# Kernel tuning notes

Hardware: AMD Instinct MI355X
Metric: run time of the kernel (lower is better)

Reference implementation:

```python
import jax, jax.numpy as jnp
import numpy as np

B, BANDS, N, IN_C, F, C = 4096, 5, 30, 512, 128, 9

def setup_inputs() -> dict:
    key = jax.random.key(0)
    ks = jax.random.split(key, 10)
    def glorot(k, shape):
        lim = float(np.sqrt(6.0 / (shape[0] + shape[-1])))
        return jax.random.uniform(k, shape, jnp.float32, -lim, lim)
    return {
        "real": jax.random.normal(ks[0], (B, N, IN_C), jnp.float32),
        "imag": jax.random.normal(ks[1], (B, N, IN_C), jnp.float32),
        "graph": jax.random.normal(ks[2], (B, BANDS, N, N), jnp.float32),
        "W1": glorot(ks[3], (IN_C, F)),
        "b1": jnp.zeros((F,), jnp.float32),
        "W2": glorot(ks[4], (F, F)),
        "b2": jnp.zeros((F,), jnp.float32),
        "Wlin": glorot(ks[5], (F, 1)),
        "blin": jnp.zeros((1,), jnp.float32),
        "Wconv": glorot(ks[6], (C, N)),  # Conv1d(30, C, k=1) weight squeezed
        "bconv": jnp.zeros((C,), jnp.float32),
    }

def _norm_adj(graph):
    # adj = mean over bands; PyG from_scipy_sparse_matrix keeps only the
    # nonzero PATTERN (edge weights are discarded in the original code).
    adj = jnp.mean(graph, axis=1)                       # [B, N, N]
    A = (adj != 0).astype(jnp.float32)
    eye = jnp.eye(A.shape[-1], dtype=jnp.float32)
    A_hat = jnp.where(eye > 0, 1.0, A)                  # add remaining self-loops
    deg = A_hat.sum(-1)                                 # [B, N]
    dinv = jnp.where(deg > 0, jax.lax.rsqrt(deg), 0.0)
    return dinv[..., :, None] * A_hat * dinv[..., None, :]  # D^-1/2 (A+I) D^-1/2

def reference(real, imag, graph, W1, b1, W2, b2, Wlin, blin, Wconv, bconv):
    An = _norm_adj(graph)                               # [B, N, N]
    # GCNConv layer 1: propagate(x @ W) + bias, then ReLU (dropout = eval identity)
    h = jnp.einsum('bnm,bmf->bnf', An, real @ W1) + b1
    h = jax.nn.relu(h)
    # GCNConv layer 2
    h = jnp.einsum('bnm,bmf->bnf', An, h @ W2) + b2
    h = jax.nn.relu(h)
    # lin: [B, N, F] -> [B, N], relu, then Conv1d(30->C, k=1) over length-1 axis
    x = jax.nn.relu((h @ Wlin + blin).squeeze(-1))      # [B, N]
    out = x @ Wconv.T + bconv                           # [B, C]
    return out
```

## Files before the change

kernel.cpp:

```cpp
#include <hip/hip_runtime.h>
#include <cstdint>

#define B_SZ 4096
#define NN   30
#define INC  512
#define FF   128
#define CC   9

__global__ __launch_bounds__(128) void k_norm_adj(const float* __restrict__ graph,
                                                  float* __restrict__ An) {
  __shared__ float Ah[NN * NN];
  __shared__ float dinv[NN];
  const int b = blockIdx.x;
  const float* g = graph + (long)b * 5 * NN * NN;
  for (int e = threadIdx.x; e < NN * NN; e += 128) {
    float s = g[e] + g[e + 900] + g[e + 1800] + g[e + 2700] + g[e + 3600];
    float mean = s * 0.2f;
    int i = e / NN;
    int j = e - i * NN;
    Ah[e] = (mean != 0.0f || i == j) ? 1.0f : 0.0f;
  }
  __syncthreads();
  if (threadIdx.x < NN) {
    float d = 0.f;
#pragma unroll
    for (int j = 0; j < NN; ++j) d += Ah[threadIdx.x * NN + j];
    dinv[threadIdx.x] = (d > 0.f) ? (1.0f / sqrtf(d)) : 0.0f;
  }
  __syncthreads();
  float* ob = An + (long)b * NN * NN;
  for (int e = threadIdx.x; e < NN * NN; e += 128) {
    int i = e / NN;
    int j = e - i * NN;
    ob[e] = Ah[e] * dinv[i] * dinv[j];
  }
}

template <int K>
__global__ __launch_bounds__(256) void k_gemm(const float* __restrict__ A,
                                              const float* __restrict__ B,
                                              float* __restrict__ C) {
  constexpr int BM = 128, BN = 128, BK = 16;
  __shared__ float As[BK][BM + 4];
  __shared__ float Bs[BK][BN + 4];
  const int tid = threadIdx.x;
  const int tx = tid & 15;
  const int ty = tid >> 4;
  const long m0 = (long)blockIdx.x * BM;

  float acc[8][8];
#pragma unroll
  for (int i = 0; i < 8; ++i)
#pragma unroll
    for (int j = 0; j < 8; ++j) acc[i][j] = 0.f;

  for (int k0 = 0; k0 < K; k0 += BK) {
#pragma unroll
    for (int it = 0; it < 2; ++it) {
      int idx = tid + 256 * it;
      int arow = idx >> 2;
      int akq = idx & 3;
      float4 av = *(const float4*)(A + (m0 + arow) * (long)K + k0 + akq * 4);
      As[akq * 4 + 0][arow] = av.x;
      As[akq * 4 + 1][arow] = av.y;
      As[akq * 4 + 2][arow] = av.z;
      As[akq * 4 + 3][arow] = av.w;
      int brow = idx >> 5;
      int bc4 = idx & 31;
      float4 bv = *(const float4*)(B + (long)(k0 + brow) * BN + bc4 * 4);
      *(float4*)&Bs[brow][bc4 * 4] = bv;
    }
    __syncthreads();
#pragma unroll
    for (int k = 0; k < BK; ++k) {
      float4 a0 = *(const float4*)&As[k][ty * 8];
      float4 a1 = *(const float4*)&As[k][ty * 8 + 4];
      float4 b0 = *(const float4*)&Bs[k][tx * 4];
      float4 b1 = *(const float4*)&Bs[k][64 + tx * 4];
      float a[8] = {a0.x, a0.y, a0.z, a0.w, a1.x, a1.y, a1.z, a1.w};
      float b[8] = {b0.x, b0.y, b0.z, b0.w, b1.x, b1.y, b1.z, b1.w};
#pragma unroll
      for (int i = 0; i < 8; ++i)
#pragma unroll
        for (int j = 0; j < 8; ++j) acc[i][j] = fmaf(a[i], b[j], acc[i][j]);
    }
    __syncthreads();
  }

#pragma unroll
  for (int i = 0; i < 8; ++i) {
    long row = m0 + ty * 8 + i;
    float4 lo = make_float4(acc[i][0], acc[i][1], acc[i][2], acc[i][3]);
    float4 hi = make_float4(acc[i][4], acc[i][5], acc[i][6], acc[i][7]);
    *(float4*)(C + row * BN + tx * 4) = lo;
    *(float4*)(C + row * BN + 64 + tx * 4) = hi;
  }
}

__global__ __launch_bounds__(128) void k_prop1(const float* __restrict__ An,
                                               const float* __restrict__ Y,
                                               const float* __restrict__ b1,
                                               float* __restrict__ H1) {
  const int b = blockIdx.x;
  const int f = threadIdx.x;
  const float* Yb = Y + (long)b * NN * FF + f;
  float y[NN];
#pragma unroll
  for (int m = 0; m < NN; ++m) y[m] = Yb[m * FF];
  const float* Ab = An + (long)b * NN * NN;
  const float bias = b1[f];
  float* Hb = H1 + (long)b * NN * FF + f;
#pragma unroll 1
  for (int i = 0; i < NN; ++i) {
    float acc = bias;
#pragma unroll
    for (int m = 0; m < NN; ++m) acc = fmaf(Ab[i * NN + m], y[m], acc);
    Hb[i * FF] = fmaxf(acc, 0.f);
  }
}

__global__ __launch_bounds__(128) void k_final(const float* __restrict__ An,
                                               const float* __restrict__ T,
                                               const float* __restrict__ b2,
                                               const float* __restrict__ Wlin,
                                               const float* __restrict__ blin,
                                               const float* __restrict__ Wconv,
                                               const float* __restrict__ bconv,
                                               float* __restrict__ out) {
  __shared__ float partial[2][NN];
  __shared__ float xs[NN];
  const int b = blockIdx.x;
  const int f = threadIdx.x;
  const int wave = f >> 6;
  const int lane = f & 63;
  const float* Tb = T + (long)b * NN * FF + f;
  float t[NN];
#pragma unroll
  for (int m = 0; m < NN; ++m) t[m] = Tb[m * FF];
  const float* Ab = An + (long)b * NN * NN;
  const float bias = b2[f];
  const float wl = Wlin[f];
#pragma unroll 1
  for (int i = 0; i < NN; ++i) {
    float acc = bias;
#pragma unroll
    for (int m = 0; m < NN; ++m) acc = fmaf(Ab[i * NN + m], t[m], acc);
    float c = fmaxf(acc, 0.f) * wl;
#pragma unroll
    for (int off = 32; off > 0; off >>= 1) c += __shfl_down(c, off, 64);
    if (lane == 0) partial[wave][i] = c;
  }
  __syncthreads();
  if (f < NN) {
    float x = partial[0][f] + partial[1][f] + blin[0];
    xs[f] = fmaxf(x, 0.f);
  }
  __syncthreads();
  if (f < CC) {
    float o = bconv[f];
#pragma unroll
    for (int i = 0; i < NN; ++i) o = fmaf(xs[i], Wconv[f * NN + i], o);
    out[(long)b * CC + f] = o;
  }
}

extern "C" void kernel_launch(void* const* d_in, const int* in_sizes, int n_in,
                              void* d_out, int out_size, void* d_ws, size_t ws_size,
                              hipStream_t stream) {
  const float* real  = (const float*)d_in[0];
  const float* graph = (const float*)d_in[2];
  const float* W1    = (const float*)d_in[3];
  const float* b1    = (const float*)d_in[4];
  const float* W2    = (const float*)d_in[5];
  const float* b2    = (const float*)d_in[6];
  const float* Wlin  = (const float*)d_in[7];
  const float* blin  = (const float*)d_in[8];
  const float* Wconv = (const float*)d_in[9];
  const float* bconv = (const float*)d_in[10];
  float* out = (float*)d_out;

  float* An = (float*)d_ws;
  float* Y  = An + (long)B_SZ * NN * NN;
  float* H1 = Y + (long)B_SZ * NN * FF;
  float* T  = Y;

  const int M = B_SZ * NN;

  k_norm_adj<<<B_SZ, 128, 0, stream>>>(graph, An);
  k_gemm<INC><<<M / 128, 256, 0, stream>>>(real, W1, Y);
  k_prop1<<<B_SZ, 128, 0, stream>>>(An, Y, b1, H1);
  k_gemm<FF><<<M / 128, 256, 0, stream>>>(H1, W2, T);
  k_final<<<B_SZ, 128, 0, stream>>>(An, T, b2, Wlin, blin, Wconv, bconv, out);
}
```

Baseline: 758.1 us.

## Replace FP32 SIMT GEMMs with split-bf16 MFMA GEMMs (3-pass emulated fp32)

Both dense GEMMs move from scalar FMA loops to MFMA bf16 matrix instructions. Each fp32 value is split into high and low bf16 halves, and three MFMA passes (hi*hi, lo*hi, hi*lo) approximate fp32 accuracy. Weights are pre-split and transposed by a small prep kernel each call, while activations are split on the fly when loaded into LDS. This targets the FP32 ALU bound of the large 122880x512x128 GEMM. It adds conversion work and scalar uncoalesced output stores, and gives slightly lower precision than true fp32.

```diff
diff --git a/kernel.cpp b/kernel.cpp
--- a/kernel.cpp
+++ b/kernel.cpp
@@ -6,6 +6,18 @@
 #define INC  512
 #define FF   128
 #define CC   9
+
+typedef short short8 __attribute__((ext_vector_type(8)));
+typedef float f32x4 __attribute__((ext_vector_type(4)));
+typedef unsigned short us4 __attribute__((ext_vector_type(4)));
+
+__device__ inline void split_bf16(float x, unsigned short& hi, unsigned short& lo) {
+  uint32_t bits = __float_as_uint(x);
+  hi = (unsigned short)(bits >> 16);
+  float hif = __uint_as_float(((uint32_t)hi) << 16);
+  float r = x - hif;
+  lo = (unsigned short)(__float_as_uint(r) >> 16);
+}
 
 __global__ __launch_bounds__(128) void k_norm_adj(const float* __restrict__ graph,
                                                   float* __restrict__ An) {
@@ -36,64 +48,107 @@
   }
 }
 
+__global__ __launch_bounds__(256) void k_prep_w(const float* __restrict__ W,
+                                                unsigned short* __restrict__ Wth,
+                                                unsigned short* __restrict__ Wtl,
+                                                int K) {
+  int idx = blockIdx.x * 256 + threadIdx.x;
+  if (idx >= K * FF) return;
+  int k = idx >> 7;
+  int n = idx & 127;
+  unsigned short h, l;
+  split_bf16(W[idx], h, l);
+  Wth[n * K + k] = h;
+  Wtl[n * K + k] = l;
+}
+
 template <int K>
-__global__ __launch_bounds__(256) void k_gemm(const float* __restrict__ A,
-                                              const float* __restrict__ B,
-                                              float* __restrict__ C) {
-  constexpr int BM = 128, BN = 128, BK = 16;
-  __shared__ float As[BK][BM + 4];
-  __shared__ float Bs[BK][BN + 4];
+__global__ __launch_bounds__(256) void k_gemm_mfma(const float* __restrict__ A,
+                                                   const unsigned short* __restrict__ Bth,
+                                                   const unsigned short* __restrict__ Btl,
+                                                   float* __restrict__ C) {
+  constexpr int BK = 32;
+  constexpr int LDT = 48;
+  __shared__ unsigned short Ash[128 * LDT];
+  __shared__ unsigned short Asl[128 * LDT];
+  __shared__ unsigned short Bsh[128 * LDT];
+  __shared__ unsigned short Bsl[128 * LDT];
+
   const int tid = threadIdx.x;
-  const int tx = tid & 15;
-  const int ty = tid >> 4;
-  const long m0 = (long)blockIdx.x * BM;
-
-  float acc[8][8];
-#pragma unroll
-  for (int i = 0; i < 8; ++i)
-#pragma unroll
-    for (int j = 0; j < 8; ++j) acc[i][j] = 0.f;
+  const int wave = tid >> 6;
+  const int lane = tid & 63;
+  const int wrow = (wave >> 1) * 64;
+  const int wcol = (wave & 1) * 64;
+  const int fr = lane & 15;
+  const int fq = lane >> 4;
+  const long m0 = (long)blockIdx.x * 128;
+
+  f32x4 acc[4][4];
+#pragma unroll
+  for (int i = 0; i < 4; ++i)
+#pragma unroll
+    for (int j = 0; j < 4; ++j) acc[i][j] = (f32x4){0.f, 0.f, 0.f, 0.f};
 
   for (int k0 = 0; k0 < K; k0 += BK) {
 #pragma unroll
-    for (int it = 0; it < 2; ++it) {
-      int idx = tid + 256 * it;
-      int arow = idx >> 2;
-      int akq = idx & 3;
-      float4 av = *(const float4*)(A + (m0 + arow) * (long)K + k0 + akq * 4);
-      As[akq * 4 + 0][arow] = av.x;
-      As[akq * 4 + 1][arow] = av.y;
-      As[akq * 4 + 2][arow] = av.z;
-      As[akq * 4 + 3][arow] = av.w;
-      int brow = idx >> 5;
-      int bc4 = idx & 31;
-      float4 bv = *(const float4*)(B + (long)(k0 + brow) * BN + bc4 * 4);
-      *(float4*)&Bs[brow][bc4 * 4] = bv;
+    for (int it = 0; it < 4; ++it) {
+      int f = tid + it * 256;
+      int row = f >> 3;
+      int kq = f & 7;
+      float4 v = *(const float4*)(A + (m0 + row) * (long)K + k0 + kq * 4);
+      us4 h, l;
+      split_bf16(v.x, ((unsigned short*)&h)[0], ((unsigned short*)&l)[0]);
+      split_bf16(v.y, ((unsigned short*)&h)[1], ((unsigned short*)&l)[1]);
+      split_bf16(v.z, ((unsigned short*)&h)[2], ((unsigned short*)&l)[2]);
+      split_bf16(v.w, ((unsigned short*)&h)[3], ((unsigned short*)&l)[3]);
+      *(us4*)(Ash + row * LDT + kq * 4) = h;
+      *(us4*)(Asl + row * LDT + kq * 4) = l;
+    }
+#pragma unroll
+    for (int it = 0; it < 4; ++it) {
+      int f = tid + it * 256;
+      int n = f >> 3;
+      int kq = f & 7;
+      us4 vh = *(const us4*)(Bth + (long)n * K + k0 + kq * 4);
+      us4 vl = *(const us4*)(Btl + (long)n * K + k0 + kq * 4);
+      *(us4*)(Bsh + n * LDT + kq * 4) = vh;
+      *(us4*)(Bsl + n * LDT + kq * 4) = vl;
     }
     __syncthreads();
-#pragma unroll
-    for (int k = 0; k < BK; ++k) {
-      float4 a0 = *(const float4*)&As[k][ty * 8];
-      float4 a1 = *(const float4*)&As[k][ty * 8 + 4];
-      float4 b0 = *(const float4*)&Bs[k][tx * 4];
-      float4 b1 = *(const float4*)&Bs[k][64 + tx * 4];
-      float a[8] = {a0.x, a0.y, a0.z, a0.w, a1.x, a1.y, a1.z, a1.w};
-      float b[8] = {b0.x, b0.y, b0.z, b0.w, b1.x, b1.y, b1.z, b1.w};
-#pragma unroll
-      for (int i = 0; i < 8; ++i)
-#pragma unroll
-        for (int j = 0; j < 8; ++j) acc[i][j] = fmaf(a[i], b[j], acc[i][j]);
+
+    short8 bh[4], bl[4];
+#pragma unroll
+    for (int ct = 0; ct < 4; ++ct) {
+      int n = wcol + ct * 16 + fr;
+      bh[ct] = *(const short8*)(Bsh + n * LDT + fq * 8);
+      bl[ct] = *(const short8*)(Bsl + n * LDT + fq * 8);
+    }
+#pragma unroll
+    for (int rt = 0; rt < 4; ++rt) {
+      int m = wrow + rt * 16 + fr;
+      short8 ah = *(const short8*)(Ash + m * LDT + fq * 8);
+      short8 al = *(const short8*)(Asl + m * LDT + fq * 8);
+#pragma unroll
+      for (int ct = 0; ct < 4; ++ct) {
+        acc[rt][ct] = __builtin_amdgcn_mfma_f32_16x16x32_bf16(ah, bh[ct], acc[rt][ct], 0, 0, 0);
+        acc[rt][ct] = __builtin_amdgcn_mfma_f32_16x16x32_bf16(al, bh[ct], acc[rt][ct], 0, 0, 0);
+        acc[rt][ct] = __builtin_amdgcn_mfma_f32_16x16x32_bf16(ah, bl[ct], acc[rt][ct], 0, 0, 0);
+      }
     }
     __syncthreads();
   }
 
 #pragma unroll
-  for (int i = 0; i < 8; ++i) {
-    long row = m0 + ty * 8 + i;
-    float4 lo = make_float4(acc[i][0], acc[i][1], acc[i][2], acc[i][3]);
-    float4 hi = make_float4(acc[i][4], acc[i][5], acc[i][6], acc[i][7]);
-    *(float4*)(C + row * BN + tx * 4) = lo;
-    *(float4*)(C + row * BN + 64 + tx * 4) = hi;
+  for (int rt = 0; rt < 4; ++rt) {
+#pragma unroll
+    for (int ct = 0; ct < 4; ++ct) {
+      int col = wcol + ct * 16 + fr;
+#pragma unroll
+      for (int r = 0; r < 4; ++r) {
+        long row = m0 + wrow + rt * 16 + fq * 4 + r;
+        C[row * FF + col] = acc[rt][ct][r];
+      }
+    }
   }
 }
 
@@ -182,13 +237,19 @@
   float* An = (float*)d_ws;
   float* Y  = An + (long)B_SZ * NN * NN;
   float* H1 = Y + (long)B_SZ * NN * FF;
-  float* T  = Y;
+  unsigned short* W1th = (unsigned short*)(H1 + (long)B_SZ * NN * FF);
+  unsigned short* W1tl = W1th + INC * FF;
+  unsigned short* W2th = W1tl + INC * FF;
+  unsigned short* W2tl = W2th + FF * FF;
+  float* T = Y;
 
   const int M = B_SZ * NN;
 
   k_norm_adj<<<B_SZ, 128, 0, stream>>>(graph, An);
-  k_gemm<INC><<<M / 128, 256, 0, stream>>>(real, W1, Y);
+  k_prep_w<<<(INC * FF + 255) / 256, 256, 0, stream>>>(W1, W1th, W1tl, INC);
+  k_prep_w<<<(FF * FF + 255) / 256, 256, 0, stream>>>(W2, W2th, W2tl, FF);
+  k_gemm_mfma<INC><<<M / 128, 256, 0, stream>>>(real, W1th, W1tl, Y);
   k_prop1<<<B_SZ, 128, 0, stream>>>(An, Y, b1, H1);
-  k_gemm<FF><<<M / 128, 256, 0, stream>>>(H1, W2, T);
+  k_gemm_mfma<FF><<<M / 128, 256, 0, stream>>>(H1, W2th, W2tl, T);
   k_final<<<B_SZ, 128, 0, stream>>>(An, T, b2, Wlin, blin, Wconv, bconv, out);
 }
```

New measurement: 632.0 us. 1.2x faster.
